# Kernel optimization log

Measured on AMD Instinct MI355X. Metric: run time of the kernel, lower is better.

Reference implementation:

```python
import jax, jax.numpy as jnp
import numpy as np

B, T, D, H = 8192, 128, 16, 32
EPS = 1e-5  # BatchNorm1d default eps (eval mode, running stats)


def setup_inputs() -> dict:
    key = jax.random.key(0)
    ks = iter(jax.random.split(key, 64))

    def nrm(shape, s=0.1):
        return jax.random.normal(next(ks), shape, jnp.float32) * s

    inp = {}
    inp["S"] = nrm((B, T, D), 1.0)
    inp["g_S"] = nrm((B, T), 1.0)
    inp["times"] = jnp.linspace(0.0, 1.0, T, dtype=jnp.float32)
    inp["payoff_T"] = nrm((B,), 1.0)
    inp["delta_T"] = nrm((B, D), 1.0)
    # init_hidden: uniform(-0.1, 0.1), shape [num_layers=2, B, H]
    inp["h_price0"] = jax.random.uniform(next(ks), (2, B, H), jnp.float32, -0.1, 0.1)
    inp["h_delta0"] = jax.random.uniform(next(ks), (2, B, H), jnp.float32, -0.1, 0.1)
    # params for price net (prefix p_, out_dim=1) and delta net (prefix d_, out_dim=D)
    for pfx, out_dim in (("p", 1), ("d", D)):
        inp[pfx + "_Wih0"] = nrm((3 * H, 2 * D))
        inp[pfx + "_Whh0"] = nrm((3 * H, H))
        inp[pfx + "_bih0"] = nrm((3 * H,))
        inp[pfx + "_bhh0"] = nrm((3 * H,))
        inp[pfx + "_Wih1"] = nrm((3 * H, H))
        inp[pfx + "_Whh1"] = nrm((3 * H, H))
        inp[pfx + "_bih1"] = nrm((3 * H,))
        inp[pfx + "_bhh1"] = nrm((3 * H,))
        inp[pfx + "_embW"] = nrm((H, H))
        inp[pfx + "_embB"] = nrm((H,))
        inp[pfx + "_bng"] = jnp.ones((H,), jnp.float32)
        inp[pfx + "_bnb"] = jnp.zeros((H,), jnp.float32)
        inp[pfx + "_bnm"] = nrm((H,))
        inp[pfx + "_bnv"] = jax.random.uniform(next(ks), (H,), jnp.float32, 0.5, 1.5)
        inp[pfx + "_outW"] = nrm((out_dim, H))
        inp[pfx + "_outB"] = nrm((out_dim,))
    return inp


def _gru_cell(x, h, Wih, Whh, bih, bhh):
    # PyTorch GRU cell, gate order (r, z, n)
    gi = x @ Wih.T + bih
    gh = h @ Whh.T + bhh
    ir, iz, inn = jnp.split(gi, 3, axis=-1)
    hr, hz, hn = jnp.split(gh, 3, axis=-1)
    r = jax.nn.sigmoid(ir + hr)
    z = jax.nn.sigmoid(iz + hz)
    n = jnp.tanh(inn + r * hn)
    return (1.0 - z) * n + z * h


def _head(y, Wemb, bemb, g, b, m, v, Wout, bout, sig):
    # Linear -> BatchNorm1d (eval, running stats) -> SiLU -> Linear [-> Sigmoid]
    e = y @ Wemb.T + bemb
    e = (e - m) * jax.lax.rsqrt(v + EPS) * g + b
    e = e * jax.nn.sigmoid(e)  # SiLU
    o = e @ Wout.T + bout
    return jax.nn.sigmoid(o) if sig else o


def reference(S, g_S, times, payoff_T, delta_T, h_price0, h_delta0,
              p_Wih0, p_Whh0, p_bih0, p_bhh0, p_Wih1, p_Whh1, p_bih1, p_bhh1,
              p_embW, p_embB, p_bng, p_bnb, p_bnm, p_bnv, p_outW, p_outB,
              d_Wih0, d_Whh0, d_bih0, d_bhh0, d_Wih1, d_Whh1, d_bih1, d_bhh1,
              d_embW, d_embB, d_bng, d_bnb, d_bnm, d_bnv, d_outW, d_outB):
    # X = cat([S, g_S expanded to d]) -> [B, T, 2D]
    gS = jnp.broadcast_to(g_S[..., None], S.shape)
    X = jnp.concatenate([S, gS], axis=-1)
    Xr = jnp.swapaxes(X, 0, 1)[::-1]  # [T, B, 2D], time reversed (loop goes t=T-1..0)

    def step(carry, xt):
        hp0, hp1, hd0, hd1 = carry
        hp0 = _gru_cell(xt, hp0, p_Wih0, p_Whh0, p_bih0, p_bhh0)
        hp1 = _gru_cell(hp0, hp1, p_Wih1, p_Whh1, p_bih1, p_bhh1)
        hd0 = _gru_cell(xt, hd0, d_Wih0, d_Whh0, d_bih0, d_bhh0)
        hd1 = _gru_cell(hd0, hd1, d_Wih1, d_Whh1, d_bih1, d_bhh1)
        return (hp0, hp1, hd0, hd1), (hp1, hd1)

    carry0 = (h_price0[0], h_price0[1], h_delta0[0], h_delta0[1])
    _, (Yp, Yd) = jax.lax.scan(step, carry0, Xr)
    # flip time back to forward order: outputs were collected for t=T-1..0
    Yp = jnp.swapaxes(Yp[::-1], 0, 1)  # [B, T, H]
    Yd = jnp.swapaxes(Yd[::-1], 0, 1)  # [B, T, H]
    prices = _head(Yp, p_embW, p_embB, p_bng, p_bnb, p_bnm, p_bnv, p_outW, p_outB, False)  # [B,T,1]
    deltas = _head(Yd, d_embW, d_embB, d_bng, d_bnb, d_bnm, d_bnv, d_outW, d_outB, True)   # [B,T,D]
    return (prices, deltas)
```

## Files before the change

### kernel.cpp

```cpp
#include <hip/hip_runtime.h>
#include <hip/hip_bf16.h>
#include <stdint.h>

#define DI __device__ __forceinline__

typedef float f32x4 __attribute__((ext_vector_type(4)));
typedef short bf16x8 __attribute__((ext_vector_type(8)));

constexpr int BB = 8192, TT = 128, DD = 16, HH = 32;
constexpr float kEPS = 1e-5f;
constexpr float kLOG2E = 1.44269504088896340736f;

DI float rcpf_(float x) { return __builtin_amdgcn_rcpf(x); }
DI float exp2f_(float x) { return __builtin_amdgcn_exp2f(x); }
DI float sig_pre(float acc) { return rcpf_(1.0f + exp2f_(acc)); }
DI float sigm(float x) { return rcpf_(1.0f + exp2f_(-kLOG2E * x)); }

DI uint32_t cvtpk(float lo, float hi) {
  uint32_t r;
  asm("v_cvt_pk_bf16_f32 %0, %1, %2" : "=v"(r) : "v"(lo), "v"(hi));
  return r;
}

DI f32x4 mfma_(bf16x8 a, bf16x8 b, f32x4 c) {
  return __builtin_amdgcn_mfma_f32_16x16x32_bf16(a, b, c, 0, 0, 0);
}

union U4 { uint4 q; bf16x8 v; };

__global__ void prep_net(const float* Wih0, const float* Whh0,
                         const float* bih0, const float* bhh0,
                         const float* Wih1, const float* Whh1,
                         const float* bih1, const float* bhh1,
                         const float* embW, const float* embB,
                         const float* bng, const float* bnb,
                         const float* bnm, const float* bnv,
                         const float* outW, const float* outB,
                         int outDim, uint8_t* wsbase) {
  int tid = threadIdx.x;
  uint16_t* W = (uint16_t*)wsbase;
  float* bias = (float*)(wsbase + 27648);
  auto cvt = [](float f) -> uint16_t {
    union { float f; uint32_t u; } v; v.f = f;
    uint32_t u = v.u;
    return (uint16_t)((u + 0x7FFF + ((u >> 16) & 1)) >> 16);
  };
  for (int idx = tid; idx < 27 * 64; idx += 256) {
    int tile = idx >> 6, l = idx & 63, cc = l & 15, gg = l >> 4;
    uint16_t* dst = W + (size_t)idx * 8;
    if (tile < 24) {
      const float* mats[4] = {Wih0, Whh0, Wih1, Whh1};
      const float* src = mats[tile / 6];
      int sub = tile % 6;
      int row = sub * 16 + cc;
      float sc = (sub < 4) ? -kLOG2E : 2.0f * kLOG2E;
#pragma unroll
      for (int j = 0; j < 8; ++j) dst[j] = cvt(src[row * 32 + 8 * gg + j] * sc);
    } else if (tile < 26) {
      int row = (tile - 24) * 16 + cc;
      float a = bng[row] * rsqrtf(bnv[row] + kEPS);
#pragma unroll
      for (int j = 0; j < 8; ++j) dst[j] = cvt(embW[row * 32 + 8 * gg + j] * a);
    } else {
      int rrow = (cc < outDim) ? cc : 0;
      float sc = (cc < outDim) ? 1.0f : 0.0f;
#pragma unroll
      for (int j = 0; j < 8; ++j) dst[j] = cvt(outW[rrow * 32 + 8 * gg + j] * sc);
    }
  }
  for (int idx = tid; idx < 304; idx += 256) {
    int tile = idx >> 4, n = idx & 15;
    float v;
    if (tile < 8) {
      if (tile < 4)      v = (bih0[tile * 16 + n] + bhh0[tile * 16 + n]) * (-kLOG2E);
      else if (tile < 6) v = bih0[64 + (tile - 4) * 16 + n] * (2.0f * kLOG2E);
      else               v = bhh0[64 + (tile - 6) * 16 + n] * (2.0f * kLOG2E);
    } else if (tile < 16) {
      int tt = tile - 8;
      if (tt < 4)        v = (bih1[tt * 16 + n] + bhh1[tt * 16 + n]) * (-kLOG2E);
      else if (tt < 6)   v = bih1[64 + (tt - 4) * 16 + n] * (2.0f * kLOG2E);
      else               v = bhh1[64 + (tt - 6) * 16 + n] * (2.0f * kLOG2E);
    } else if (tile < 18) {
      int nn = (tile - 16) * 16 + n;
      float a = bng[nn] * rsqrtf(bnv[nn] + kEPS);
      v = a * (embB[nn] - bnm[nn]) + bnb[nn];
    } else {
      v = (n < outDim) ? outB[n] : 0.0f;
    }
    bias[idx] = v;
  }
}

__global__ __launch_bounds__(128, 2) void rnn_fused(
    const float* __restrict__ S, const float* __restrict__ gS,
    const float* __restrict__ hp0, const float* __restrict__ hd0,
    const uint8_t* __restrict__ ws, float* __restrict__ out) {
  const int tid = threadIdx.x, lane = tid & 63, wid = tid >> 6;
  const int net = blockIdx.x & 1;
  const int b0 = (blockIdx.x >> 1) * 16;
  const int c = lane & 15, g = lane >> 4;

  const uint16_t* W = (const uint16_t*)(ws + net * 32768);
  const float* bias = (const float*)(ws + net * 32768 + 27648);
  const float* hsrc = net ? hd0 : hp0;

  __shared__ uint4 ring0[8][64];
  __shared__ volatile int flags[2];
  if (tid < 2) flags[tid] = 0;
  __syncthreads();

  auto waitGE = [&](int idx, int target) {
    if (flags[idx] >= target) return;
    do { __builtin_amdgcn_s_sleep(1); } while (flags[idx] < target);
  };

  const int addr0 = ((lane & 15) | ((lane & 16) << 1)) << 2;
  const int addr1 = addr0 + 64;
  const bool lo32 = lane < 32;
  auto regroup = [&](const float (&v)[8]) -> bf16x8 {
    int P0 = (int)cvtpk(v[0], v[1]), P1 = (int)cvtpk(v[2], v[3]);
    int Q0 = (int)cvtpk(v[4], v[5]), Q1 = (int)cvtpk(v[6], v[7]);
    union { uint32_t u[4]; bf16x8 r; } t;
    int a, b;
    a = __builtin_amdgcn_ds_bpermute(addr0, P0);
    b = __builtin_amdgcn_ds_bpermute(addr0, Q0);
    t.u[0] = lo32 ? a : b;
    a = __builtin_amdgcn_ds_bpermute(addr0, P1);
    b = __builtin_amdgcn_ds_bpermute(addr0, Q1);
    t.u[1] = lo32 ? a : b;
    a = __builtin_amdgcn_ds_bpermute(addr1, P0);
    b = __builtin_amdgcn_ds_bpermute(addr1, Q0);
    t.u[2] = lo32 ? a : b;
    a = __builtin_amdgcn_ds_bpermute(addr1, P1);
    b = __builtin_amdgcn_ds_bpermute(addr1, Q1);
    t.u[3] = lo32 ? a : b;
    return t.r;
  };

  auto gruStep = [&](const bf16x8 (&Wi)[6], const bf16x8 (&Wh)[6],
                     const f32x4 (&Bb)[8], bf16x8 xf, bf16x8 hf,
                     float (&hC)[8]) {
    f32x4 r0 = mfma_(Wi[0], xf, Bb[0]); r0 = mfma_(Wh[0], hf, r0);
    f32x4 r1 = mfma_(Wi[1], xf, Bb[1]); r1 = mfma_(Wh[1], hf, r1);
    f32x4 z0 = mfma_(Wi[2], xf, Bb[2]); z0 = mfma_(Wh[2], hf, z0);
    f32x4 z1 = mfma_(Wi[3], xf, Bb[3]); z1 = mfma_(Wh[3], hf, z1);
    f32x4 ni0 = mfma_(Wi[4], xf, Bb[4]);
    f32x4 ni1 = mfma_(Wi[5], xf, Bb[5]);
    f32x4 nh0 = mfma_(Wh[4], hf, Bb[6]);
    f32x4 nh1 = mfma_(Wh[5], hf, Bb[7]);
#pragma unroll
    for (int r = 0; r < 4; ++r) {
      float rg0 = sig_pre(r0[r]), rg1 = sig_pre(r1[r]);
      float zg0 = sig_pre(z0[r]), zg1 = sig_pre(z1[r]);
      float w0 = ni0[r] + rg0 * nh0[r];
      float w1 = ni1[r] + rg1 * nh1[r];
      float n0 = 1.0f - 2.0f * rcpf_(1.0f + exp2f_(w0));
      float n1 = 1.0f - 2.0f * rcpf_(1.0f + exp2f_(w1));
      hC[r]     = n0 + zg0 * (hC[r]     - n0);
      hC[4 + r] = n1 + zg1 * (hC[4 + r] - n1);
    }
  };

  auto mkB = [&](const float* row) -> bf16x8 {
    f32x4 a = *(const f32x4*)(row);
    f32x4 b = *(const f32x4*)(row + 4);
    union { uint32_t u[4]; bf16x8 v; } t;
    t.u[0] = cvtpk(a[0], a[1]); t.u[1] = cvtpk(a[2], a[3]);
    t.u[2] = cvtpk(b[0], b[1]); t.u[3] = cvtpk(b[2], b[3]);
    return t.v;
  };

  if (wid == 0) {
    bf16x8 Wi[6], Wh[6];
#pragma unroll
    for (int t = 0; t < 6; ++t) {
      Wi[t] = *(const bf16x8*)(W + ((0 + t) * 64 + lane) * 8);
      Wh[t] = *(const bf16x8*)(W + ((6 + t) * 64 + lane) * 8);
    }
    f32x4 Bb[8];
#pragma unroll
    for (int t = 0; t < 8; ++t)
      Bb[t] = *(const f32x4*)(bias + t * 16 + 4 * g);

    float h0C[8];
#pragma unroll
    for (int r = 0; r < 4; ++r) {
      h0C[r]     = hsrc[(size_t)(b0 + c) * HH + 4 * g + r];
      h0C[4 + r] = hsrc[(size_t)(b0 + c) * HH + 16 + 4 * g + r];
    }
    bf16x8 h0B = mkB(hsrc + (size_t)(b0 + c) * HH + 8 * g);

    auto mkX = [&](f32x4 sa, f32x4 sb, float gsv) -> bf16x8 {
      uint32_t pkg = cvtpk(gsv, gsv);
      union { uint32_t u[4]; bf16x8 v; } t;
      uint32_t p0 = cvtpk(sa[0], sa[1]), p1 = cvtpk(sa[2], sa[3]);
      uint32_t p2 = cvtpk(sb[0], sb[1]), p3 = cvtpk(sb[2], sb[3]);
      t.u[0] = lo32 ? p0 : pkg;
      t.u[1] = lo32 ? p1 : pkg;
      t.u[2] = lo32 ? p2 : pkg;
      t.u[3] = lo32 ? p3 : pkg;
      return t.v;
    };

    const float* Sbase  = S  + (size_t)(b0 + c) * TT * DD + 8 * (g & 1);
    const float* gSbase = gS + (size_t)(b0 + c) * TT;

    f32x4 sa0 = *(const f32x4*)(Sbase + (size_t)(TT - 1) * DD);
    f32x4 sb0 = *(const f32x4*)(Sbase + (size_t)(TT - 1) * DD + 4);
    float gv0 = gSbase[TT - 1];
    f32x4 sa1 = *(const f32x4*)(Sbase + (size_t)(TT - 2) * DD);
    f32x4 sb1 = *(const f32x4*)(Sbase + (size_t)(TT - 2) * DD + 4);
    float gv1 = gSbase[TT - 2];

#pragma unroll 2
    for (int i = 0; i < TT; ++i) {
      int tn = TT - 3 - i; if (tn < 0) tn = 0;
      const float* p = Sbase + (size_t)tn * DD;
      f32x4 san = *(const f32x4*)p, sbn = *(const f32x4*)(p + 4);
      float gvn = gSbase[tn];

      bf16x8 xB = mkX(sa0, sb0, gv0);
      gruStep(Wi, Wh, Bb, xB, h0B, h0C);
      h0B = regroup(h0C);

      if (i >= 7) waitGE(1, i - 7);
      asm volatile("" ::: "memory");
      { U4 u; u.v = h0B; ring0[i & 7][lane] = u.q; }
      asm volatile("s_waitcnt lgkmcnt(0)" ::: "memory");
      if (lane == 0) flags[0] = i + 1;

      sa0 = sa1; sb0 = sb1; gv0 = gv1;
      sa1 = san; sb1 = sbn; gv1 = gvn;
    }
  } else {
    bf16x8 Wi[6], Wh[6], We0, We1, Wo;
#pragma unroll
    for (int t = 0; t < 6; ++t) {
      Wi[t] = *(const bf16x8*)(W + ((12 + t) * 64 + lane) * 8);
      Wh[t] = *(const bf16x8*)(W + ((18 + t) * 64 + lane) * 8);
    }
    We0 = *(const bf16x8*)(W + (24 * 64 + lane) * 8);
    We1 = *(const bf16x8*)(W + (25 * 64 + lane) * 8);
    Wo  = *(const bf16x8*)(W + (26 * 64 + lane) * 8);
    f32x4 Bb[8];
#pragma unroll
    for (int t = 0; t < 8; ++t)
      Bb[t] = *(const f32x4*)(bias + (8 + t) * 16 + 4 * g);
    const f32x4 Be0 = *(const f32x4*)(bias + 16 * 16 + 4 * g);
    const f32x4 Be1 = *(const f32x4*)(bias + 17 * 16 + 4 * g);
    const f32x4 Bo  = *(const f32x4*)(bias + 18 * 16 + 4 * g);

    float h1C[8];
#pragma unroll
    for (int r = 0; r < 4; ++r) {
      h1C[r]     = hsrc[((size_t)BB + b0 + c) * HH + 4 * g + r];
      h1C[4 + r] = hsrc[((size_t)BB + b0 + c) * HH + 16 + 4 * g + r];
    }
    bf16x8 h1B = mkB(hsrc + ((size_t)BB + b0 + c) * HH + 8 * g);

    auto head = [&](bf16x8 h1f, int th) {
      f32x4 e0 = mfma_(We0, h1f, Be0);
      f32x4 e1 = mfma_(We1, h1f, Be1);
      float es[8];
#pragma unroll
      for (int r = 0; r < 4; ++r) {
        float a = e0[r], b = e1[r];
        es[r]     = a * sigm(a);
        es[4 + r] = b * sigm(b);
      }
      bf16x8 ef = regroup(es);
      f32x4 o = mfma_(Wo, ef, Bo);
      if (net == 0) {
        if (lane < 16) out[(size_t)(b0 + c) * TT + th] = o[0];
      } else {
        f32x4 so;
#pragma unroll
        for (int r = 0; r < 4; ++r) so[r] = sigm(o[r]);
        *(f32x4*)(out + (size_t)BB * TT +
                  ((size_t)(b0 + c) * TT + th) * DD + 4 * g) = so;
      }
    };

#pragma unroll 1
    for (int i = 0; i < TT; ++i) {
      waitGE(0, i + 1);
      asm volatile("" ::: "memory");
      U4 u; u.q = ring0[i & 7][lane];
      asm volatile("s_waitcnt lgkmcnt(0)" ::: "memory");
      if (lane == 0) flags[1] = i + 1;

      bf16x8 h1prev = h1B;
      gruStep(Wi, Wh, Bb, u.v, h1B, h1C);
      if (i > 0) head(h1prev, TT - i);
      h1B = regroup(h1C);
    }
    head(h1B, 0);
  }
}

extern "C" void kernel_launch(void* const* d_in, const int* in_sizes, int n_in,
                              void* d_out, int out_size, void* d_ws,
                              size_t ws_size, hipStream_t stream) {
  const float* S   = (const float*)d_in[0];
  const float* gS  = (const float*)d_in[1];
  const float* hp0 = (const float*)d_in[5];
  const float* hd0 = (const float*)d_in[6];
  uint8_t* ws = (uint8_t*)d_ws;

  prep_net<<<1, 256, 0, stream>>>(
      (const float*)d_in[7],  (const float*)d_in[8],  (const float*)d_in[9],
      (const float*)d_in[10], (const float*)d_in[11], (const float*)d_in[12],
      (const float*)d_in[13], (const float*)d_in[14], (const float*)d_in[15],
      (const float*)d_in[16], (const float*)d_in[17], (const float*)d_in[18],
      (const float*)d_in[19], (const float*)d_in[20], (const float*)d_in[21],
      (const float*)d_in[22], 1, ws);
  prep_net<<<1, 256, 0, stream>>>(
      (const float*)d_in[23], (const float*)d_in[24], (const float*)d_in[25],
      (const float*)d_in[26], (const float*)d_in[27], (const float*)d_in[28],
      (const float*)d_in[29], (const float*)d_in[30], (const float*)d_in[31],
      (const float*)d_in[32], (const float*)d_in[33], (const float*)d_in[34],
      (const float*)d_in[35], (const float*)d_in[36], (const float*)d_in[37],
      (const float*)d_in[38], 16, ws + 32768);

  rnn_fused<<<dim3((BB / 16) * 2), dim3(128), 0, stream>>>(S, gS, hp0, hd0,
                                                           ws, (float*)d_out);
}
```

Baseline: 162.0 us.

## Split GRU layer1 and output head into separate waves with two-step batching

The output head moves out of the layer-1 wave into a third wavefront, fed through a second LDS ring buffer with its own flags, so each block now runs a three-stage pipeline of 192 threads. Both GRU waves now process two timesteps per flag handshake, which halves the synchronisation traffic. The gate maths is rewritten to merge the z-gate sigmoid and the tanh into one reciprocal, cutting transcendental ops per step. The cost is more threads per block, a second ring buffer in LDS, and possible occupancy and register pressure changes from the new launch bounds.

```diff
diff --git a/kernel.cpp b/kernel.cpp
--- a/kernel.cpp
+++ b/kernel.cpp
@@ -13,7 +13,6 @@
 
 DI float rcpf_(float x) { return __builtin_amdgcn_rcpf(x); }
 DI float exp2f_(float x) { return __builtin_amdgcn_exp2f(x); }
-DI float sig_pre(float acc) { return rcpf_(1.0f + exp2f_(acc)); }
 DI float sigm(float x) { return rcpf_(1.0f + exp2f_(-kLOG2E * x)); }
 
 DI uint32_t cvtpk(float lo, float hi) {
@@ -91,7 +90,7 @@
   }
 }
 
-__global__ __launch_bounds__(128, 2) void rnn_fused(
+__global__ __launch_bounds__(192, 3) void rnn_fused(
     const float* __restrict__ S, const float* __restrict__ gS,
     const float* __restrict__ hp0, const float* __restrict__ hd0,
     const uint8_t* __restrict__ ws, float* __restrict__ out) {
@@ -105,8 +104,9 @@
   const float* hsrc = net ? hd0 : hp0;
 
   __shared__ uint4 ring0[8][64];
-  __shared__ volatile int flags[2];
-  if (tid < 2) flags[tid] = 0;
+  __shared__ uint4 ring1[8][64];
+  __shared__ volatile int flags[4];
+  if (tid < 4) flags[tid] = 0;
   __syncthreads();
 
   auto waitGE = [&](int idx, int target) {
@@ -150,14 +150,19 @@
     f32x4 nh1 = mfma_(Wh[5], hf, Bb[7]);
 #pragma unroll
     for (int r = 0; r < 4; ++r) {
-      float rg0 = sig_pre(r0[r]), rg1 = sig_pre(r1[r]);
-      float zg0 = sig_pre(z0[r]), zg1 = sig_pre(z1[r]);
+      float rg0 = rcpf_(1.0f + exp2f_(r0[r]));
+      float rg1 = rcpf_(1.0f + exp2f_(r1[r]));
       float w0 = ni0[r] + rg0 * nh0[r];
       float w1 = ni1[r] + rg1 * nh1[r];
-      float n0 = 1.0f - 2.0f * rcpf_(1.0f + exp2f_(w0));
-      float n1 = 1.0f - 2.0f * rcpf_(1.0f + exp2f_(w1));
-      hC[r]     = n0 + zg0 * (hC[r]     - n0);
-      hC[4 + r] = n1 + zg1 * (hC[4 + r] - n1);
+      float En0 = exp2f_(w0), En1 = exp2f_(w1);
+      float Ez0 = exp2f_(z0[r]), Ez1 = exp2f_(z1[r]);
+      float hv0 = hC[r], hv1 = hC[4 + r];
+      float num0 = (hv0 - Ez0) + En0 * (hv0 + Ez0);
+      float num1 = (hv1 - Ez1) + En1 * (hv1 + Ez1);
+      float den0 = (1.0f + En0) * (1.0f + Ez0);
+      float den1 = (1.0f + En1) * (1.0f + Ez1);
+      hC[r]     = num0 * rcpf_(den0);
+      hC[4 + r] = num1 * rcpf_(den1);
     }
   };
 
@@ -204,59 +209,93 @@
 
     const float* Sbase  = S  + (size_t)(b0 + c) * TT * DD + 8 * (g & 1);
     const float* gSbase = gS + (size_t)(b0 + c) * TT;
-
-    f32x4 sa0 = *(const f32x4*)(Sbase + (size_t)(TT - 1) * DD);
-    f32x4 sb0 = *(const f32x4*)(Sbase + (size_t)(TT - 1) * DD + 4);
-    float gv0 = gSbase[TT - 1];
-    f32x4 sa1 = *(const f32x4*)(Sbase + (size_t)(TT - 2) * DD);
-    f32x4 sb1 = *(const f32x4*)(Sbase + (size_t)(TT - 2) * DD + 4);
-    float gv1 = gSbase[TT - 2];
-
-#pragma unroll 2
-    for (int i = 0; i < TT; ++i) {
-      int tn = TT - 3 - i; if (tn < 0) tn = 0;
-      const float* p = Sbase + (size_t)tn * DD;
-      f32x4 san = *(const f32x4*)p, sbn = *(const f32x4*)(p + 4);
-      float gvn = gSbase[tn];
-
-      bf16x8 xB = mkX(sa0, sb0, gv0);
-      gruStep(Wi, Wh, Bb, xB, h0B, h0C);
+    auto loadX = [&](int t, f32x4& a, f32x4& b, float& gv) {
+      const float* p = Sbase + (size_t)t * DD;
+      a = *(const f32x4*)p; b = *(const f32x4*)(p + 4); gv = gSbase[t];
+    };
+
+    f32x4 ca0, cb0, ca1, cb1, na0, nb0, na1, nb1;
+    float cg0, cg1, ng0, ng1;
+    loadX(TT - 1, ca0, cb0, cg0);
+    loadX(TT - 2, ca1, cb1, cg1);
+
+#pragma unroll 1
+    for (int ip = 0; ip < TT / 2; ++ip) {
+      int tn0 = TT - 3 - 2 * ip; if (tn0 < 0) tn0 = 0;
+      int tn1 = TT - 4 - 2 * ip; if (tn1 < 0) tn1 = 0;
+      loadX(tn0, na0, nb0, ng0);
+      loadX(tn1, na1, nb1, ng1);
+
+      bf16x8 x0 = mkX(ca0, cb0, cg0);
+      gruStep(Wi, Wh, Bb, x0, h0B, h0C);
       h0B = regroup(h0C);
-
-      if (i >= 7) waitGE(1, i - 7);
+      U4 f0v; f0v.v = h0B;
+      bf16x8 x1 = mkX(ca1, cb1, cg1);
+      gruStep(Wi, Wh, Bb, x1, h0B, h0C);
+      h0B = regroup(h0C);
+      U4 f1v; f1v.v = h0B;
+
+      if (ip >= 4) waitGE(1, 2 * ip - 6);
       asm volatile("" ::: "memory");
-      { U4 u; u.v = h0B; ring0[i & 7][lane] = u.q; }
+      ring0[(2 * ip) & 7][lane]     = f0v.q;
+      ring0[(2 * ip + 1) & 7][lane] = f1v.q;
       asm volatile("s_waitcnt lgkmcnt(0)" ::: "memory");
-      if (lane == 0) flags[0] = i + 1;
-
-      sa0 = sa1; sb0 = sb1; gv0 = gv1;
-      sa1 = san; sb1 = sbn; gv1 = gvn;
-    }
-  } else {
-    bf16x8 Wi[6], Wh[6], We0, We1, Wo;
+      if (lane == 0) flags[0] = 2 * ip + 2;
+
+      ca0 = na0; cb0 = nb0; cg0 = ng0;
+      ca1 = na1; cb1 = nb1; cg1 = ng1;
+    }
+  } else if (wid == 1) {
+    bf16x8 Wi[6], Wh[6];
 #pragma unroll
     for (int t = 0; t < 6; ++t) {
       Wi[t] = *(const bf16x8*)(W + ((12 + t) * 64 + lane) * 8);
       Wh[t] = *(const bf16x8*)(W + ((18 + t) * 64 + lane) * 8);
     }
-    We0 = *(const bf16x8*)(W + (24 * 64 + lane) * 8);
-    We1 = *(const bf16x8*)(W + (25 * 64 + lane) * 8);
-    Wo  = *(const bf16x8*)(W + (26 * 64 + lane) * 8);
     f32x4 Bb[8];
 #pragma unroll
     for (int t = 0; t < 8; ++t)
       Bb[t] = *(const f32x4*)(bias + (8 + t) * 16 + 4 * g);
+
+    float h1C[8];
+#pragma unroll
+    for (int r = 0; r < 4; ++r) {
+      h1C[r]     = hsrc[((size_t)BB + b0 + c) * HH + 4 * g + r];
+      h1C[4 + r] = hsrc[((size_t)BB + b0 + c) * HH + 16 + 4 * g + r];
+    }
+    bf16x8 h1B = mkB(hsrc + ((size_t)BB + b0 + c) * HH + 8 * g);
+
+#pragma unroll 1
+    for (int ip = 0; ip < TT / 2; ++ip) {
+      waitGE(0, 2 * ip + 2);
+      asm volatile("" ::: "memory");
+      U4 u0, u1;
+      u0.q = ring0[(2 * ip) & 7][lane];
+      u1.q = ring0[(2 * ip + 1) & 7][lane];
+      asm volatile("s_waitcnt lgkmcnt(0)" ::: "memory");
+      if (lane == 0) flags[1] = 2 * ip + 2;
+
+      gruStep(Wi, Wh, Bb, u0.v, h1B, h1C);
+      h1B = regroup(h1C);
+      U4 f0v; f0v.v = h1B;
+      gruStep(Wi, Wh, Bb, u1.v, h1B, h1C);
+      h1B = regroup(h1C);
+      U4 f1v; f1v.v = h1B;
+
+      if (ip >= 4) waitGE(3, 2 * ip - 6);
+      asm volatile("" ::: "memory");
+      ring1[(2 * ip) & 7][lane]     = f0v.q;
+      ring1[(2 * ip + 1) & 7][lane] = f1v.q;
+      asm volatile("s_waitcnt lgkmcnt(0)" ::: "memory");
+      if (lane == 0) flags[2] = 2 * ip + 2;
+    }
+  } else {
+    bf16x8 We0 = *(const bf16x8*)(W + (24 * 64 + lane) * 8);
+    bf16x8 We1 = *(const bf16x8*)(W + (25 * 64 + lane) * 8);
+    bf16x8 Wo  = *(const bf16x8*)(W + (26 * 64 + lane) * 8);
     const f32x4 Be0 = *(const f32x4*)(bias + 16 * 16 + 4 * g);
     const f32x4 Be1 = *(const f32x4*)(bias + 17 * 16 + 4 * g);
     const f32x4 Bo  = *(const f32x4*)(bias + 18 * 16 + 4 * g);
-
-    float h1C[8];
-#pragma unroll
-    for (int r = 0; r < 4; ++r) {
-      h1C[r]     = hsrc[((size_t)BB + b0 + c) * HH + 4 * g + r];
-      h1C[4 + r] = hsrc[((size_t)BB + b0 + c) * HH + 16 + 4 * g + r];
-    }
-    bf16x8 h1B = mkB(hsrc + ((size_t)BB + b0 + c) * HH + 8 * g);
 
     auto head = [&](bf16x8 h1f, int th) {
       f32x4 e0 = mfma_(We0, h1f, Be0);
@@ -282,19 +321,18 @@
     };
 
 #pragma unroll 1
-    for (int i = 0; i < TT; ++i) {
-      waitGE(0, i + 1);
+    for (int ip = 0; ip < TT / 2; ++ip) {
+      waitGE(2, 2 * ip + 2);
       asm volatile("" ::: "memory");
-      U4 u; u.q = ring0[i & 7][lane];
+      U4 u0, u1;
+      u0.q = ring1[(2 * ip) & 7][lane];
+      u1.q = ring1[(2 * ip + 1) & 7][lane];
       asm volatile("s_waitcnt lgkmcnt(0)" ::: "memory");
-      if (lane == 0) flags[1] = i + 1;
-
-      bf16x8 h1prev = h1B;
-      gruStep(Wi, Wh, Bb, u.v, h1B, h1C);
-      if (i > 0) head(h1prev, TT - i);
-      h1B = regroup(h1C);
-    }
-    head(h1B, 0);
+      if (lane == 0) flags[3] = 2 * ip + 2;
+
+      head(u0.v, TT - 1 - 2 * ip);
+      head(u1.v, TT - 2 - 2 * ip);
+    }
   }
 }
 
@@ -322,6 +360,6 @@
       (const float*)d_in[35], (const float*)d_in[36], (const float*)d_in[37],
       (const float*)d_in[38], 16, ws + 32768);
 
-  rnn_fused<<<dim3((BB / 16) * 2), dim3(128), 0, stream>>>(S, gS, hp0, hd0,
+  rnn_fused<<<dim3((BB / 16) * 2), dim3(192), 0, stream>>>(S, gS, hp0, hd0,
                                                            ws, (float*)d_out);
 }
```

Measured after the change: 162.3 us. No clear change (+0.2%).
